# Performance work log

Measured on AMD Instinct MI355X. Metric: run time of the kernel, lower is better.

Reference implementation:

```python
import jax, jax.numpy as jnp
import numpy as np

B = 256
D_MODEL = 2048
EXPAND = 4
D_INNER = EXPAND * D_MODEL  # 8192
D_STATE = 16
D_CONV = 4
DT_RANK = (D_MODEL + 15) // 16  # 128


def setup_inputs() -> dict:
    key = jax.random.key(0)
    ks = jax.random.split(key, 12)
    s = 0.02  # weight scale
    return {
        "x": jax.random.normal(ks[0], (B, 1, D_MODEL), jnp.float32),
        "conv_state": jax.random.normal(ks[1], (B, D_INNER, D_CONV), jnp.float32),
        "ssm_state": jax.random.normal(ks[2], (B, D_INNER, D_STATE), jnp.float32),
        "W_in": jax.random.normal(ks[3], (2 * D_INNER, D_MODEL), jnp.float32) * s,
        "conv_w": jax.random.normal(ks[4], (D_INNER, D_CONV), jnp.float32) * s,
        "conv_b": jax.random.normal(ks[5], (D_INNER,), jnp.float32) * s,
        "W_xproj": jax.random.normal(ks[6], (DT_RANK + 2 * D_STATE, D_INNER), jnp.float32) * s,
        "W_dt": jax.random.normal(ks[7], (D_INNER, DT_RANK), jnp.float32) * s,
        "b_dt": jax.random.normal(ks[8], (D_INNER,), jnp.float32) * s,
        "A_log": jnp.log(jax.random.uniform(ks[9], (D_INNER, D_STATE), jnp.float32, 0.5, 8.0)),
        "D_param": jax.random.normal(ks[10], (D_INNER,), jnp.float32),
        "W_out": jax.random.normal(ks[11], (D_MODEL, D_INNER), jnp.float32) * s,
    }


def reference(x, conv_state, ssm_state, W_in, conv_w, conv_b, W_xproj,
              W_dt, b_dt, A_log, D_param, W_out):
    # x: (B, 1, d_model) -> single-token Mamba.step
    xz = x[:, 0, :] @ W_in.T                      # (B, 2*d_inner)
    xi, z = jnp.split(xz, 2, axis=-1)             # (B, d_inner) each

    # depthwise conv state update (roll left, append new token)
    conv_state = jnp.concatenate([conv_state[:, :, 1:], xi[:, :, None]], axis=-1)
    xc = jnp.sum(conv_state * conv_w[None, :, :], axis=-1) + conv_b  # (B, d_inner)
    xc = jax.nn.silu(xc)

    # input-dependent SSM params
    x_db = xc @ W_xproj.T                          # (B, dt_rank + 2*d_state)
    dt = x_db[:, :DT_RANK]
    Bm = x_db[:, DT_RANK:DT_RANK + D_STATE]        # (B, d_state)
    Cm = x_db[:, DT_RANK + D_STATE:]               # (B, d_state)
    dt = jax.nn.softplus(dt @ W_dt.T + b_dt)       # (B, d_inner)

    # discretize + single-step state update
    A = -jnp.exp(A_log)                            # (d_inner, d_state)
    dA = jnp.exp(dt[:, :, None] * A[None])         # (B, d_inner, d_state)
    dB = dt[:, :, None] * Bm[:, None, :]           # (B, d_inner, d_state)
    ssm_state = ssm_state * dA + xc[:, :, None] * dB

    y = jnp.einsum('bdn,bn->bd', ssm_state, Cm) + D_param * xc
    y = y * jax.nn.silu(z)
    out = (y @ W_out.T)[:, None, :]                # (B, 1, d_model)
    return out, conv_state, ssm_state
```

## Files before the change

### kernel.cpp

```cpp
#include <hip/hip_runtime.h>
#include <hip/hip_bf16.h>

typedef __attribute__((ext_vector_type(8))) short   sv8;
typedef __attribute__((ext_vector_type(8))) __bf16  bfv8;
typedef __attribute__((ext_vector_type(4))) float   f32x4;

__device__ __forceinline__ short f2bf(float f) {
  union { float f; unsigned u; } v; v.f = f;
  unsigned r = v.u + 0x7fffu + ((v.u >> 16) & 1u);
  return (short)(r >> 16);
}

__device__ __forceinline__ f32x4 mfma16x16x32(sv8 a, sv8 b, f32x4 c) {
  return __builtin_amdgcn_mfma_f32_16x16x32_bf16(
      __builtin_bit_cast(bfv8, a), __builtin_bit_cast(bfv8, b), c, 0, 0, 0);
}

__device__ __forceinline__ float silu(float x) { return x / (1.f + __expf(-x)); }

template<int EPI>
__global__ __launch_bounds__(256) void gemm_bt(
    const float* __restrict__ A, const float* __restrict__ B, float* __restrict__ C,
    const float* __restrict__ bias, int lda, int ldb, int ldc, int kIters,
    int kStride, long cSlice)
{
  __shared__ short As[128 * 72];
  __shared__ short Bs[128 * 72];
  const int tid = threadIdx.x;
  A += (long)blockIdx.z * kStride;
  B += (long)blockIdx.z * kStride;
  C += (long)blockIdx.z * cSlice;
  const int rowA0 = blockIdx.y * 128, colB0 = blockIdx.x * 128;
  const int c4 = tid & 15, r0 = tid >> 4;
  const int wave = tid >> 6, lane = tid & 63;
  const int wm = (wave >> 1) * 64, wn = (wave & 1) * 64;
  const int lrow = lane & 15, lq = lane >> 4;
  f32x4 acc[4][4] = {};

  for (int kb = 0; kb < kIters; ++kb) {
    const int k0 = kb * 64;
#pragma unroll
    for (int i = 0; i < 8; ++i) {
      const int r = r0 + 16 * i;
      const float4 va = *(const float4*)&A[(long)(rowA0 + r) * lda + k0 + c4 * 4];
      const float4 vb = *(const float4*)&B[(long)(colB0 + r) * ldb + k0 + c4 * 4];
      short4 sa; sa.x = f2bf(va.x); sa.y = f2bf(va.y); sa.z = f2bf(va.z); sa.w = f2bf(va.w);
      short4 sb; sb.x = f2bf(vb.x); sb.y = f2bf(vb.y); sb.z = f2bf(vb.z); sb.w = f2bf(vb.w);
      *(short4*)&As[r * 72 + c4 * 4] = sa;
      *(short4*)&Bs[r * 72 + c4 * 4] = sb;
    }
    __syncthreads();
#pragma unroll
    for (int ks = 0; ks < 2; ++ks) {
      const int kk = ks * 32 + lq * 8;
      sv8 af[4], bfr[4];
#pragma unroll
      for (int s = 0; s < 4; ++s) {
        af[s]  = *(const sv8*)&As[(wm + s * 16 + lrow) * 72 + kk];
        bfr[s] = *(const sv8*)&Bs[(wn + s * 16 + lrow) * 72 + kk];
      }
#pragma unroll
      for (int sm = 0; sm < 4; ++sm)
#pragma unroll
        for (int sn = 0; sn < 4; ++sn)
          acc[sm][sn] = mfma16x16x32(af[sm], bfr[sn], acc[sm][sn]);
    }
    __syncthreads();
  }
#pragma unroll
  for (int sm = 0; sm < 4; ++sm) {
    const int row = rowA0 + wm + sm * 16 + lq * 4;
#pragma unroll
    for (int sn = 0; sn < 4; ++sn) {
      const int col = colB0 + wn + sn * 16 + lrow;
#pragma unroll
      for (int r = 0; r < 4; ++r) {
        float v = acc[sm][sn][r];
        if (EPI == 1) { v += bias[col]; v = (v > 20.f) ? v : log1pf(__expf(v)); }
        C[(long)(row + r) * ldc + col] = v;
      }
    }
  }
}

__global__ __launch_bounds__(256) void conv_step(
    const float* __restrict__ xz, const float* __restrict__ cs_in,
    const float* __restrict__ conv_w, const float* __restrict__ conv_b,
    float* __restrict__ cs_out, float* __restrict__ xc)
{
  const long i = (long)blockIdx.x * 256 + threadIdx.x;
  const int b = (int)(i >> 13), d = (int)(i & 8191);
  const float4 c = *(const float4*)&cs_in[i * 4];
  const float4 w = *(const float4*)&conv_w[(long)d * 4];
  const float xi = xz[(long)b * 16384 + d];
  float4 nc; nc.x = c.y; nc.y = c.z; nc.z = c.w; nc.w = xi;
  *(float4*)&cs_out[i * 4] = nc;
  const float v = nc.x * w.x + nc.y * w.y + nc.z * w.z + nc.w * w.w + conv_b[d];
  xc[i] = silu(v);
}

__global__ void zero_kernel(float* p) { p[blockIdx.x * 256 + threadIdx.x] = 0.f; }

__global__ __launch_bounds__(256) void gemm_xdb(
    const float* __restrict__ xc, const float* __restrict__ W, float* __restrict__ out)
{
  __shared__ short As[256 * 72];
  __shared__ short Bs[16 * 72];
  const int tid = threadIdx.x;
  const int nt = blockIdx.x;
  const long kbase = (long)blockIdx.y * 512;
  const int c4 = tid & 15, r0 = tid >> 4;
  const int wave = tid >> 6, lane = tid & 63;
  const int lrow = lane & 15, lq = lane >> 4;
  f32x4 acc[4] = {};
  for (int kb = 0; kb < 8; ++kb) {
    const long k0 = kbase + kb * 64;
#pragma unroll
    for (int i = 0; i < 16; ++i) {
      const int r = r0 + 16 * i;
      const float4 v = *(const float4*)&xc[(long)r * 8192 + k0 + c4 * 4];
      short4 s; s.x = f2bf(v.x); s.y = f2bf(v.y); s.z = f2bf(v.z); s.w = f2bf(v.w);
      *(short4*)&As[r * 72 + c4 * 4] = s;
    }
    {
      const float4 v = *(const float4*)&W[(long)(nt * 16 + r0) * 8192 + k0 + c4 * 4];
      short4 s; s.x = f2bf(v.x); s.y = f2bf(v.y); s.z = f2bf(v.z); s.w = f2bf(v.w);
      *(short4*)&Bs[r0 * 72 + c4 * 4] = s;
    }
    __syncthreads();
#pragma unroll
    for (int ks = 0; ks < 2; ++ks) {
      const int kk = ks * 32 + lq * 8;
      const sv8 bfr = *(const sv8*)&Bs[lrow * 72 + kk];
#pragma unroll
      for (int s = 0; s < 4; ++s) {
        const sv8 af = *(const sv8*)&As[((wave * 4 + s) * 16 + lrow) * 72 + kk];
        acc[s] = mfma16x16x32(af, bfr, acc[s]);
      }
    }
    __syncthreads();
  }
  const int n = nt * 16 + lrow;
#pragma unroll
  for (int s = 0; s < 4; ++s) {
    const int m0 = (wave * 4 + s) * 16 + lq * 4;
#pragma unroll
    for (int r = 0; r < 4; ++r) atomicAdd(&out[(long)(m0 + r) * 160 + n], acc[s][r]);
  }
}

__global__ __launch_bounds__(256) void ssm_step(
    const float* __restrict__ ssm_in, const float* __restrict__ x_db,
    const float* __restrict__ dtv, const float* __restrict__ xcw,
    const float* __restrict__ xz, const float* __restrict__ A_log,
    const float* __restrict__ D_param, float* __restrict__ ssm_out, float* __restrict__ y)
{
  const long t = (long)blockIdx.x * 256 + threadIdx.x;
  const long bd = t >> 2; const int sq = (int)(t & 3);
  const int b = (int)(bd >> 13), d = (int)(bd & 8191);
  const float dt = dtv[bd];
  const float xc = xcw[bd];
  const float4 al = *(const float4*)&A_log[(long)d * 16 + sq * 4];
  const float4 st = *(const float4*)&ssm_in[bd * 16 + sq * 4];
  const float4 Bv = *(const float4*)&x_db[(long)b * 160 + 128 + sq * 4];
  const float4 Cv = *(const float4*)&x_db[(long)b * 160 + 144 + sq * 4];
  const float xdt = xc * dt;
  float4 ns;
  ns.x = st.x * __expf(dt * -__expf(al.x)) + xdt * Bv.x;
  ns.y = st.y * __expf(dt * -__expf(al.y)) + xdt * Bv.y;
  ns.z = st.z * __expf(dt * -__expf(al.z)) + xdt * Bv.z;
  ns.w = st.w * __expf(dt * -__expf(al.w)) + xdt * Bv.w;
  *(float4*)&ssm_out[bd * 16 + sq * 4] = ns;
  float part = ns.x * Cv.x + ns.y * Cv.y + ns.z * Cv.z + ns.w * Cv.w;
  part += __shfl_xor(part, 1);
  part += __shfl_xor(part, 2);
  if (sq == 0) {
    const float z = xz[(long)b * 16384 + 8192 + d];
    float yv = part + D_param[d] * xc;
    y[bd] = yv * silu(z);
  }
}

__global__ __launch_bounds__(256) void reduce8(const float* __restrict__ p, float* __restrict__ out)
{
  const long i = (long)blockIdx.x * 256 + threadIdx.x;
  float4 s = {0.f, 0.f, 0.f, 0.f};
#pragma unroll
  for (int j = 0; j < 8; ++j) {
    const float4 v = *(const float4*)&p[(long)j * 524288 + i * 4];
    s.x += v.x; s.y += v.y; s.z += v.z; s.w += v.w;
  }
  *(float4*)&out[i * 4] = s;
}

extern "C" void kernel_launch(void* const* d_in, const int* in_sizes, int n_in,
                              void* d_out, int out_size, void* d_ws, size_t ws_size,
                              hipStream_t stream) {
  const float* x        = (const float*)d_in[0];
  const float* conv_in  = (const float*)d_in[1];
  const float* ssm_in   = (const float*)d_in[2];
  const float* W_in     = (const float*)d_in[3];
  const float* conv_w   = (const float*)d_in[4];
  const float* conv_b   = (const float*)d_in[5];
  const float* W_xproj  = (const float*)d_in[6];
  const float* W_dt     = (const float*)d_in[7];
  const float* b_dt     = (const float*)d_in[8];
  const float* A_log    = (const float*)d_in[9];
  const float* D_param  = (const float*)d_in[10];
  const float* W_out    = (const float*)d_in[11];

  float* out      = (float*)d_out;
  float* conv_out = out + 524288;
  float* ssm_out  = out + 8912896;

  float* ws   = (float*)d_ws;
  float* xz   = ws;
  float* xcw  = ws + 4194304;
  float* x_db = ws + 6291456;
  float* dtv  = ws + 6332416;
  float* yv   = ws + 8429568;
  float* partials = xz;

  gemm_bt<0><<<dim3(128, 2, 1), 256, 0, stream>>>(x, W_in, xz, nullptr, 2048, 2048, 16384, 32, 0, 0);
  conv_step<<<8192, 256, 0, stream>>>(xz, conv_in, conv_w, conv_b, conv_out, xcw);
  zero_kernel<<<160, 256, 0, stream>>>(x_db);
  gemm_xdb<<<dim3(10, 16), 256, 0, stream>>>(xcw, W_xproj, x_db);
  gemm_bt<1><<<dim3(64, 2, 1), 256, 0, stream>>>(x_db, W_dt, dtv, b_dt, 160, 128, 8192, 2, 0, 0);
  ssm_step<<<32768, 256, 0, stream>>>(ssm_in, x_db, dtv, xcw, xz, A_log, D_param, ssm_out, yv);
  gemm_bt<0><<<dim3(16, 2, 8), 256, 0, stream>>>(yv, W_out, partials, nullptr, 8192, 8192, 2048, 16, 1024, 524288);
  reduce8<<<512, 256, 0, stream>>>(partials, out);
}
```

Baseline: 593.7 us.

## Halve GEMM N-tile and register-prefetch next K-slice during MFMA compute

The shared gemm_bt kernel now uses a 128x64 output tile instead of 128x128, which doubles the grid size for all three GEMM launches to give more blocks across the CUs. It also loads the next K-slice of A and B into registers before the MFMA loop of the current slice, so global load latency can overlap with compute. The costs are lower reuse of the A tile (A is re-read by twice as many blocks) and higher register use for the prefetch buffers.

Result: faster. 550.5 us (-7.3%).

```diff
diff --git a/kernel.cpp b/kernel.cpp
--- a/kernel.cpp
+++ b/kernel.cpp
@@ -25,44 +25,58 @@
     int kStride, long cSlice)
 {
   __shared__ short As[128 * 72];
-  __shared__ short Bs[128 * 72];
+  __shared__ short Bs[64 * 72];
   const int tid = threadIdx.x;
   A += (long)blockIdx.z * kStride;
   B += (long)blockIdx.z * kStride;
   C += (long)blockIdx.z * cSlice;
-  const int rowA0 = blockIdx.y * 128, colB0 = blockIdx.x * 128;
+  const int rowA0 = blockIdx.y * 128, colB0 = blockIdx.x * 64;
   const int c4 = tid & 15, r0 = tid >> 4;
   const int wave = tid >> 6, lane = tid & 63;
-  const int wm = (wave >> 1) * 64, wn = (wave & 1) * 64;
+  const int wm = (wave >> 1) * 64, wn = (wave & 1) * 32;
   const int lrow = lane & 15, lq = lane >> 4;
-  f32x4 acc[4][4] = {};
+  f32x4 acc[4][2] = {};
+  float4 pa[8], pb[4];
+
+  const float* Aptr = &A[(long)(rowA0 + r0) * lda + c4 * 4];
+  const float* Bptr = &B[(long)(colB0 + r0) * ldb + c4 * 4];
+
+#pragma unroll
+  for (int i = 0; i < 8; ++i) pa[i] = *(const float4*)&Aptr[(long)(16 * i) * lda];
+#pragma unroll
+  for (int i = 0; i < 4; ++i) pb[i] = *(const float4*)&Bptr[(long)(16 * i) * ldb];
 
   for (int kb = 0; kb < kIters; ++kb) {
-    const int k0 = kb * 64;
 #pragma unroll
     for (int i = 0; i < 8; ++i) {
-      const int r = r0 + 16 * i;
-      const float4 va = *(const float4*)&A[(long)(rowA0 + r) * lda + k0 + c4 * 4];
-      const float4 vb = *(const float4*)&B[(long)(colB0 + r) * ldb + k0 + c4 * 4];
-      short4 sa; sa.x = f2bf(va.x); sa.y = f2bf(va.y); sa.z = f2bf(va.z); sa.w = f2bf(va.w);
-      short4 sb; sb.x = f2bf(vb.x); sb.y = f2bf(vb.y); sb.z = f2bf(vb.z); sb.w = f2bf(vb.w);
-      *(short4*)&As[r * 72 + c4 * 4] = sa;
-      *(short4*)&Bs[r * 72 + c4 * 4] = sb;
-    }
-    __syncthreads();
+      short4 s; s.x = f2bf(pa[i].x); s.y = f2bf(pa[i].y); s.z = f2bf(pa[i].z); s.w = f2bf(pa[i].w);
+      *(short4*)&As[(r0 + 16 * i) * 72 + c4 * 4] = s;
+    }
+#pragma unroll
+    for (int i = 0; i < 4; ++i) {
+      short4 s; s.x = f2bf(pb[i].x); s.y = f2bf(pb[i].y); s.z = f2bf(pb[i].z); s.w = f2bf(pb[i].w);
+      *(short4*)&Bs[(r0 + 16 * i) * 72 + c4 * 4] = s;
+    }
+    __syncthreads();
+    if (kb + 1 < kIters) {
+      const long ko = (long)(kb + 1) * 64;
+#pragma unroll
+      for (int i = 0; i < 8; ++i) pa[i] = *(const float4*)&Aptr[(long)(16 * i) * lda + ko];
+#pragma unroll
+      for (int i = 0; i < 4; ++i) pb[i] = *(const float4*)&Bptr[(long)(16 * i) * ldb + ko];
+    }
 #pragma unroll
     for (int ks = 0; ks < 2; ++ks) {
       const int kk = ks * 32 + lq * 8;
-      sv8 af[4], bfr[4];
-#pragma unroll
-      for (int s = 0; s < 4; ++s) {
-        af[s]  = *(const sv8*)&As[(wm + s * 16 + lrow) * 72 + kk];
-        bfr[s] = *(const sv8*)&Bs[(wn + s * 16 + lrow) * 72 + kk];
-      }
+      sv8 af[4], bfr[2];
+#pragma unroll
+      for (int s = 0; s < 4; ++s) af[s] = *(const sv8*)&As[(wm + s * 16 + lrow) * 72 + kk];
+#pragma unroll
+      for (int s = 0; s < 2; ++s) bfr[s] = *(const sv8*)&Bs[(wn + s * 16 + lrow) * 72 + kk];
 #pragma unroll
       for (int sm = 0; sm < 4; ++sm)
 #pragma unroll
-        for (int sn = 0; sn < 4; ++sn)
+        for (int sn = 0; sn < 2; ++sn)
           acc[sm][sn] = mfma16x16x32(af[sm], bfr[sn], acc[sm][sn]);
     }
     __syncthreads();
@@ -71,7 +85,7 @@
   for (int sm = 0; sm < 4; ++sm) {
     const int row = rowA0 + wm + sm * 16 + lq * 4;
 #pragma unroll
-    for (int sn = 0; sn < 4; ++sn) {
+    for (int sn = 0; sn < 2; ++sn) {
       const int col = colB0 + wn + sn * 16 + lrow;
 #pragma unroll
       for (int r = 0; r < 4; ++r) {
@@ -221,12 +235,12 @@
   float* yv   = ws + 8429568;
   float* partials = xz;
 
-  gemm_bt<0><<<dim3(128, 2, 1), 256, 0, stream>>>(x, W_in, xz, nullptr, 2048, 2048, 16384, 32, 0, 0);
+  gemm_bt<0><<<dim3(256, 2, 1), 256, 0, stream>>>(x, W_in, xz, nullptr, 2048, 2048, 16384, 32, 0, 0);
   conv_step<<<8192, 256, 0, stream>>>(xz, conv_in, conv_w, conv_b, conv_out, xcw);
   zero_kernel<<<160, 256, 0, stream>>>(x_db);
   gemm_xdb<<<dim3(10, 16), 256, 0, stream>>>(xcw, W_xproj, x_db);
-  gemm_bt<1><<<dim3(64, 2, 1), 256, 0, stream>>>(x_db, W_dt, dtv, b_dt, 160, 128, 8192, 2, 0, 0);
+  gemm_bt<1><<<dim3(128, 2, 1), 256, 0, stream>>>(x_db, W_dt, dtv, b_dt, 160, 128, 8192, 2, 0, 0);
   ssm_step<<<32768, 256, 0, stream>>>(ssm_in, x_db, dtv, xcw, xz, A_log, D_param, ssm_out, yv);
-  gemm_bt<0><<<dim3(16, 2, 8), 256, 0, stream>>>(yv, W_out, partials, nullptr, 8192, 8192, 2048, 16, 1024, 524288);
+  gemm_bt<0><<<dim3(32, 2, 8), 256, 0, stream>>>(yv, W_out, partials, nullptr, 8192, 8192, 2048, 16, 1024, 524288);
   reduce8<<<512, 256, 0, stream>>>(partials, out);
 }
```
